# Performance work log

Hardware: AMD Instinct MI355X
Metric: run time of the kernel (lower is better)

The kernel has to match this reference:

```python
import jax, jax.numpy as jnp
import numpy as np

# Model / shape constants (match init_kwargs)
D_MODEL = 256
NHEAD = 8
H_B, W_B = 16, 8       # block_size
BN_H, BN_W = 8, 8      # block_num
B = 8
N = BN_H * H_B * BN_W * W_B  # 8192
HIDDEN = int(D_MODEL * 4.0)  # mlp_ratio * d_model
LN_EPS = 1e-5


def setup_inputs() -> dict:
    key = jax.random.key(0)
    ks = jax.random.split(key, 12)
    s = 0.02
    p = {}
    p["src"] = jax.random.normal(ks[0], (B, N, D_MODEL), jnp.float32)
    p["pos"] = jax.random.normal(ks[1], (1, N, D_MODEL), jnp.float32)
    # long-range MHA params (torch in_proj_weight [3C,C], out_proj [C,C])
    p["w_in_long"] = jax.random.normal(ks[2], (3 * D_MODEL, D_MODEL), jnp.float32) * s
    p["b_in_long"] = jnp.zeros((3 * D_MODEL,), jnp.float32)
    p["w_out_long"] = jax.random.normal(ks[3], (D_MODEL, D_MODEL), jnp.float32) * s
    p["b_out_long"] = jnp.zeros((D_MODEL,), jnp.float32)
    # short-range MHA params
    p["w_in_short"] = jax.random.normal(ks[4], (3 * D_MODEL, D_MODEL), jnp.float32) * s
    p["b_in_short"] = jnp.zeros((3 * D_MODEL,), jnp.float32)
    p["w_out_short"] = jax.random.normal(ks[5], (D_MODEL, D_MODEL), jnp.float32) * s
    p["b_out_short"] = jnp.zeros((D_MODEL,), jnp.float32)
    # FFN
    p["w1"] = jax.random.normal(ks[6], (HIDDEN, D_MODEL), jnp.float32) * s
    p["b1"] = jnp.zeros((HIDDEN,), jnp.float32)
    p["w2"] = jax.random.normal(ks[7], (D_MODEL, HIDDEN), jnp.float32) * s
    p["b2"] = jnp.zeros((D_MODEL,), jnp.float32)
    # LayerNorms
    p["g1"] = jnp.ones((D_MODEL,), jnp.float32)
    p["beta1"] = jnp.zeros((D_MODEL,), jnp.float32)
    p["g2"] = jnp.ones((D_MODEL,), jnp.float32)
    p["beta2"] = jnp.zeros((D_MODEL,), jnp.float32)
    return p


def _mha(q, k, v, w_in, b_in, w_out, b_out):
    # torch nn.MultiheadAttention, inputs [L, Bt, C] (seq-first)
    L, Bt, C = q.shape
    H, Dh = NHEAD, C // NHEAD
    wq, wk, wv = jnp.split(w_in, 3, axis=0)
    bq, bk, bv = jnp.split(b_in, 3, axis=0)
    qh = (q @ wq.T + bq).reshape(L, Bt, H, Dh)
    kh = (k @ wk.T + bk).reshape(L, Bt, H, Dh)
    vh = (v @ wv.T + bv).reshape(L, Bt, H, Dh)
    scores = jnp.einsum('lbhd,mbhd->bhlm', qh, kh) / np.sqrt(Dh).astype(np.float32)
    attn = jax.nn.softmax(scores, axis=-1)
    o = jnp.einsum('bhlm,mbhd->lbhd', attn, vh).reshape(L, Bt, C)
    return o @ w_out.T + b_out


def _ln(x, g, b):
    mu = jnp.mean(x, axis=-1, keepdims=True)
    var = jnp.var(x, axis=-1, keepdims=True)
    return (x - mu) / jnp.sqrt(var + LN_EPS) * g + b


def _isa_block(src, pos, w_in_long, b_in_long, w_out_long, b_out_long,
               w_in_short, b_in_short, w_out_short, b_out_short):
    Bs, Ns, C = src.shape
    posb = jnp.broadcast_to(pos, (Bs, Ns, C))

    def to_long(x):  # [B,N,C] -> [bn_h*bn_w, B*h_b*w_b, C]
        x = x.reshape(Bs, BN_H, H_B, BN_W, W_B, C).transpose(1, 3, 0, 2, 4, 5)
        return x.reshape(BN_H * BN_W, Bs * H_B * W_B, C)

    ql = to_long(src)
    pl = to_long(posb)
    v = _mha(ql + pl, ql + pl, ql, w_in_long, b_in_long, w_out_long, b_out_long)

    def long_to_short(x):
        # faithful to torch: view(B,bn_h,h_b,bn_w,w_b,C) REINTERPRETS the flat
        # (bn_h,bn_w,B,h_b,w_b) layout, then permute(2,4,0,1,3,5)
        x = x.reshape(Bs, BN_H, H_B, BN_W, W_B, C).transpose(2, 4, 0, 1, 3, 5)
        return x.reshape(H_B * W_B, Bs * BN_H * BN_W, C)

    v = long_to_short(v)
    ps = long_to_short(pl.reshape(Bs, BN_H, H_B, BN_W, W_B, C).reshape(BN_H * BN_W, Bs * H_B * W_B, C))
    # (the above reshape round-trip is identity; keep ps derived from pl directly)
    ps = long_to_short(pl)

    out = _mha(v + ps, v + ps, v, w_in_short, b_in_short, w_out_short, b_out_short)
    # [h_b*w_b, B*bn_h*bn_w, C] -> [B, N, C]
    out = out.reshape(H_B, W_B, Bs, BN_H, BN_W, C).transpose(2, 0, 3, 1, 4, 5)
    return out.reshape(Bs, Ns, C)


def reference(src, pos, w_in_long, b_in_long, w_out_long, b_out_long,
              w_in_short, b_in_short, w_out_short, b_out_short,
              w1, b1, w2, b2, g1, beta1, g2, beta2):
    Bs, Ns, C = src.shape
    src2 = _isa_block(src, pos, w_in_long, b_in_long, w_out_long, b_out_long,
                      w_in_short, b_in_short, w_out_short, b_out_short)
    x = src + src2            # dropout is identity at eval
    x = _ln(x, g1, beta1)
    ff = (jax.nn.relu(x @ w1.T + b1)) @ w2.T + b2
    x = _ln(x + ff, g2, beta2)
    # faithful final permute+view from the torch module (layout reinterpretation)
    x = jnp.transpose(x, (0, 2, 1)).reshape(Bs, Ns, C)
    return x
```

## Files before the change

### kernel.cpp

```cpp
#include <hip/hip_runtime.h>
#include <stdint.h>

typedef unsigned short u16;
typedef unsigned int u32;
typedef __bf16 bf16x8 __attribute__((ext_vector_type(8)));
typedef float f32x4 __attribute__((ext_vector_type(4)));

#define SC_Q 0.17677669529663687f

__device__ __forceinline__ u16 f2b(float f) {
  u32 u = __float_as_uint(f);
  u = (u + 0x7fffu + ((u >> 16) & 1u)) >> 16;
  return (u16)u;
}
__device__ __forceinline__ float b2f(u16 h) {
  return __uint_as_float(((u32)h) << 16);
}
__device__ __forceinline__ u32 pack2(float a, float b) {
  return (u32)f2b(a) | ((u32)f2b(b) << 16);
}
__device__ __forceinline__ void gload_lds16(const u16* g, u16* l) {
  __builtin_amdgcn_global_load_lds(
      (const __attribute__((address_space(1))) void*)g,
      (__attribute__((address_space(3))) void*)l, 16, 0, 0);
}

__global__ void prep_weights(const float* __restrict__ wil, const float* __restrict__ wol,
                             const float* __restrict__ wis, const float* __restrict__ wos,
                             const float* __restrict__ w1, const float* __restrict__ w2,
                             u16* __restrict__ out) {
  int idx = (blockIdx.x * 256 + threadIdx.x) * 4;
  u16 r[4];
#pragma unroll
  for (int j = 0; j < 4; ++j) {
    int i = idx + j;
    float x;
    if (i < 196608)      { x = wil[i]; if (i < 65536) x *= SC_Q; }
    else if (i < 262144) { x = wol[i - 196608]; }
    else if (i < 458752) { int k = i - 262144; x = wis[k]; if (k < 65536) x *= SC_Q; }
    else if (i < 524288) { x = wos[i - 458752]; }
    else if (i < 786432) { x = w1[i - 524288]; }
    else                 { x = w2[i - 786432]; }
    r[j] = f2b(x);
  }
  *(uint2*)(out + idx) = make_uint2((u32)r[0] | ((u32)r[1] << 16),
                                    (u32)r[2] | ((u32)r[3] << 16));
}

__global__ void prep_bias(const float* __restrict__ bil, const float* __restrict__ bis,
                          float* __restrict__ out) {
  int i = blockIdx.x * 256 + threadIdx.x;
  if (i < 768)       out[i] = bil[i] * (i < 256 ? SC_Q : 1.0f);
  else if (i < 1536) { int k = i - 768; out[i] = bis[k] * (k < 256 ? SC_Q : 1.0f); }
}

__global__ void gather_long(const float* __restrict__ src, const float* __restrict__ pos,
                            u16* __restrict__ A1, u16* __restrict__ A2) {
  int gid = blockIdx.x * 256 + threadIdx.x;
  int u = gid >> 6, lane = gid & 63;
  int l = u >> 10, t = u & 1023;
  int bh = l >> 3, bw = l & 7;
  int b = t >> 7, h = (t >> 3) & 15, w = t & 7;
  int n = bh * 1024 + h * 64 + bw * 8 + w;
  float4 s4 = ((const float4*)(src + ((size_t)b * 8192 + n) * 256))[lane];
  float4 p4 = ((const float4*)(pos + (size_t)n * 256))[lane];
  ((uint2*)(A1 + (size_t)u * 256))[lane] =
      make_uint2(pack2(s4.x + p4.x, s4.y + p4.y), pack2(s4.z + p4.z, s4.w + p4.w));
  ((uint2*)(A2 + (size_t)u * 256))[lane] =
      make_uint2(pack2(s4.x, s4.y), pack2(s4.z, s4.w));
}

__global__ void gather_short(const u16* __restrict__ VL, const float* __restrict__ pos,
                             u16* __restrict__ A1s, u16* __restrict__ A2s) {
  int gid = blockIdx.x * 256 + threadIdx.x;
  int u2 = gid >> 6, lane = gid & 63;
  int s = u2 >> 9, r = u2 & 511;
  int hq = s >> 3, wq = s & 7;
  int b = r >> 6, bh = (r >> 3) & 7, bw = r & 7;
  int u = b * 8192 + bh * 1024 + hq * 64 + bw * 8 + wq;
  int l = u >> 10, t = u & 1023;
  int pbh = l >> 3, pbw = l & 7, ph = (t >> 3) & 15, pw = t & 7;
  int np = pbh * 1024 + ph * 64 + pbw * 8 + pw;
  uint2 vv = ((const uint2*)(VL + (size_t)u * 256))[lane];
  float4 p4 = ((const float4*)(pos + (size_t)np * 256))[lane];
  float v0 = b2f((u16)(vv.x & 0xffff)), v1 = b2f((u16)(vv.x >> 16));
  float v2 = b2f((u16)(vv.y & 0xffff)), v3 = b2f((u16)(vv.y >> 16));
  ((uint2*)(A1s + (size_t)u2 * 256))[lane] =
      make_uint2(pack2(v0 + p4.x, v1 + p4.y), pack2(v2 + p4.z, v3 + p4.w));
  ((uint2*)(A2s + (size_t)u2 * 256))[lane] = vv;
}

__global__ __launch_bounds__(256) void gemm128(
    const u16* __restrict__ A1, const u16* __restrict__ A2, int n_split,
    const u16* __restrict__ W, const float* __restrict__ bias,
    u16* __restrict__ C, int N, int K, int relu) {
  __shared__ __align__(16) u16 As[128 * 32];
  __shared__ __align__(16) u16 Bs[128 * 32];
  int m0 = blockIdx.y * 128, n0 = blockIdx.x * 128;
  const u16* A = (n0 < n_split) ? A1 : A2;
  int tid = threadIdx.x;
  int lane = tid & 63, wv = tid >> 6;
  int row = tid >> 2, seg = tid & 3;
  int wr = wv & 1, wc = wv >> 1;
  int r15 = lane & 15, q = lane >> 4;
  f32x4 acc[4][4];
#pragma unroll
  for (int i = 0; i < 4; ++i)
#pragma unroll
    for (int j = 0; j < 4; ++j)
#pragma unroll
      for (int r = 0; r < 4; ++r) acc[i][j][r] = 0.f;

  const u16* ag0 = A + (size_t)(m0 + row) * K + seg * 8;
  const u16* ag1 = A + (size_t)(m0 + 64 + row) * K + seg * 8;
  const u16* bg0 = W + (size_t)(n0 + row) * K + seg * 8;
  const u16* bg1 = W + (size_t)(n0 + 64 + row) * K + seg * 8;
  u16* lA0 = As + wv * 512;
  u16* lA1 = As + wv * 512 + 2048;
  u16* lB0 = Bs + wv * 512;
  u16* lB1 = Bs + wv * 512 + 2048;

  for (int k0 = 0; k0 < K; k0 += 32) {
    gload_lds16(ag0 + k0, lA0);
    gload_lds16(ag1 + k0, lA1);
    gload_lds16(bg0 + k0, lB0);
    gload_lds16(bg1 + k0, lB1);
    __syncthreads();
    bf16x8 af[4], bf[4];
#pragma unroll
    for (int i = 0; i < 4; ++i)
      af[i] = *(const bf16x8*)&As[(wr * 64 + i * 16 + r15) * 32 + q * 8];
#pragma unroll
    for (int j = 0; j < 4; ++j)
      bf[j] = *(const bf16x8*)&Bs[(wc * 64 + j * 16 + r15) * 32 + q * 8];
#pragma unroll
    for (int i = 0; i < 4; ++i)
#pragma unroll
      for (int j = 0; j < 4; ++j)
        acc[i][j] = __builtin_amdgcn_mfma_f32_16x16x32_bf16(af[i], bf[j], acc[i][j], 0, 0, 0);
    __syncthreads();
  }
#pragma unroll
  for (int j = 0; j < 4; ++j) {
    int n = n0 + wc * 64 + j * 16 + r15;
    float bb = bias[n];
#pragma unroll
    for (int i = 0; i < 4; ++i)
#pragma unroll
      for (int r = 0; r < 4; ++r) {
        int m = m0 + wr * 64 + i * 16 + q * 4 + r;
        float v = acc[i][j][r] + bb;
        if (relu) v = fmaxf(v, 0.f);
        C[(size_t)m * N + n] = f2b(v);
      }
  }
}

template <int L, int Bt>
__global__ __launch_bounds__(4 * L) void attn_mfma(const u16* __restrict__ qkv,
                                                   u16* __restrict__ O) {
  constexpr int L16 = L / 16, LP = L + 8;
  __shared__ __align__(16) u16 Ks[L * 40];
  __shared__ __align__(16) u16 VT[32 * LP];
  __shared__ __align__(16) u16 Ps[L16 * 16 * LP];
  int p = blockIdx.x, t = p >> 3, head = p & 7;
  int tid = threadIdx.x;
  {
    int r = tid >> 2, seg = tid & 3;
    const u16* base = qkv + ((size_t)r * Bt + t) * 768 + head * 32 + seg * 8;
    uint4 kvv = *(const uint4*)(base + 256);
    *(uint4*)&Ks[r * 40 + seg * 8] = kvv;
    uint4 vv = *(const uint4*)(base + 512);
    u32 wds[4] = {vv.x, vv.y, vv.z, vv.w};
#pragma unroll
    for (int e = 0; e < 4; ++e) {
      VT[(seg * 8 + e * 2 + 0) * LP + r] = (u16)(wds[e] & 0xffffu);
      VT[(seg * 8 + e * 2 + 1) * LP + r] = (u16)(wds[e] >> 16);
    }
  }
  int lane = tid & 63, w = tid >> 6;
  int r15 = lane & 15, q = lane >> 4;
  bf16x8 af = *(const bf16x8*)(qkv + ((size_t)(w * 16 + r15) * Bt + t) * 768 + head * 32 + q * 8);
  __syncthreads();
  f32x4 z = {0.f, 0.f, 0.f, 0.f};
  f32x4 s[L16];
#pragma unroll
  for (int jt = 0; jt < L16; ++jt) {
    bf16x8 bf = *(const bf16x8*)&Ks[(jt * 16 + r15) * 40 + q * 8];
    s[jt] = __builtin_amdgcn_mfma_f32_16x16x32_bf16(af, bf, z, 0, 0, 0);
  }
  float inv[4];
#pragma unroll
  for (int r = 0; r < 4; ++r) {
    float mx = s[0][r];
#pragma unroll
    for (int jt = 1; jt < L16; ++jt) mx = fmaxf(mx, s[jt][r]);
    mx = fmaxf(mx, __shfl_xor(mx, 1));
    mx = fmaxf(mx, __shfl_xor(mx, 2));
    mx = fmaxf(mx, __shfl_xor(mx, 4));
    mx = fmaxf(mx, __shfl_xor(mx, 8));
    float sum = 0.f;
#pragma unroll
    for (int jt = 0; jt < L16; ++jt) {
      float pe = __expf(s[jt][r] - mx);
      s[jt][r] = pe;
      sum += pe;
    }
    sum += __shfl_xor(sum, 1);
    sum += __shfl_xor(sum, 2);
    sum += __shfl_xor(sum, 4);
    sum += __shfl_xor(sum, 8);
    inv[r] = 1.f / sum;
  }
  int pbase = w * 16 * LP;
#pragma unroll
  for (int jt = 0; jt < L16; ++jt)
#pragma unroll
    for (int r = 0; r < 4; ++r)
      Ps[pbase + (q * 4 + r) * LP + jt * 16 + r15] = f2b(s[jt][r]);
  __syncthreads();
  f32x4 o[2] = {z, z};
#pragma unroll
  for (int kt = 0; kt < L / 32; ++kt) {
    bf16x8 ap = *(const bf16x8*)&Ps[pbase + r15 * LP + kt * 32 + q * 8];
#pragma unroll
    for (int nt = 0; nt < 2; ++nt) {
      bf16x8 bv = *(const bf16x8*)&VT[(nt * 16 + r15) * LP + kt * 32 + q * 8];
      o[nt] = __builtin_amdgcn_mfma_f32_16x16x32_bf16(ap, bv, o[nt], 0, 0, 0);
    }
  }
#pragma unroll
  for (int nt = 0; nt < 2; ++nt)
#pragma unroll
    for (int r = 0; r < 4; ++r) {
      float v = o[nt][r] * inv[r];
      size_t addr = ((size_t)(w * 16 + q * 4 + r) * Bt + t) * 256 + head * 32 + nt * 16 + r15;
      O[addr] = f2b(v);
    }
}

__global__ void ln1(const float* __restrict__ src, const u16* __restrict__ s2b,
                    const float* __restrict__ g, const float* __restrict__ be,
                    u16* __restrict__ xln) {
  int gid = blockIdx.x * 256 + threadIdx.x;
  int u2 = gid >> 6, lane = gid & 63;
  int s = u2 >> 9, r = u2 & 511;
  int hq = s >> 3, wq = s & 7;
  int b = r >> 6, bh = (r >> 3) & 7, bw = r & 7;
  int n2 = hq * 512 + bh * 64 + wq * 8 + bw;
  size_t urow = (size_t)b * 8192 + n2;
  float4 a = ((const float4*)(src + urow * 256))[lane];
  uint2 vv = ((const uint2*)(s2b + (size_t)u2 * 256))[lane];
  float v0 = a.x + b2f((u16)(vv.x & 0xffff));
  float v1 = a.y + b2f((u16)(vv.x >> 16));
  float v2 = a.z + b2f((u16)(vv.y & 0xffff));
  float v3 = a.w + b2f((u16)(vv.y >> 16));
  float s1 = v0 + v1 + v2 + v3;
  float sq = v0*v0 + v1*v1 + v2*v2 + v3*v3;
#pragma unroll
  for (int off = 32; off >= 1; off >>= 1) {
    s1 += __shfl_xor(s1, off, 64);
    sq += __shfl_xor(sq, off, 64);
  }
  float mu = s1 * (1.f / 256.f);
  float var = sq * (1.f / 256.f) - mu * mu;
  float rstd = rsqrtf(var + 1e-5f);
  float4 g4 = ((const float4*)g)[lane];
  float4 e4 = ((const float4*)be)[lane];
  float y0 = (v0 - mu) * rstd * g4.x + e4.x;
  float y1 = (v1 - mu) * rstd * g4.y + e4.y;
  float y2 = (v2 - mu) * rstd * g4.z + e4.z;
  float y3 = (v3 - mu) * rstd * g4.w + e4.w;
  ((uint2*)(xln + urow * 256))[lane] = make_uint2(pack2(y0, y1), pack2(y2, y3));
}

__global__ __launch_bounds__(256) void ln2t(const u16* __restrict__ ff, const u16* __restrict__ xln,
                                            const float* __restrict__ g, const float* __restrict__ be,
                                            float* __restrict__ out) {
  __shared__ u16 tileT[256][65];
  __shared__ float ps1[64][4];
  __shared__ float ps2[64][4];
  __shared__ float mu_s[64], rs_s[64];
  int b = blockIdx.x >> 7;
  int n0 = (blockIdx.x & 127) * 64;
  int tid = threadIdx.x;
  int i = tid >> 2, ch = tid & 3;
  size_t u = (size_t)b * 8192 + n0 + i;
  const uint4* fr = (const uint4*)(ff + u * 256 + ch * 64);
  const uint4* xr = (const uint4*)(xln + u * 256 + ch * 64);
  float s1 = 0.f, sq = 0.f;
#pragma unroll
  for (int j = 0; j < 8; ++j) {
    uint4 fv = fr[j];
    uint4 xv = xr[j];
    u32 fw[4] = {fv.x, fv.y, fv.z, fv.w};
    u32 xw[4] = {xv.x, xv.y, xv.z, xv.w};
    int cbase = ch * 64 + j * 8;
#pragma unroll
    for (int e = 0; e < 4; ++e) {
      float f0 = __uint_as_float(fw[e] << 16) + __uint_as_float(xw[e] << 16);
      float f1 = __uint_as_float(fw[e] & 0xffff0000u) + __uint_as_float(xw[e] & 0xffff0000u);
      s1 += f0 + f1; sq += f0 * f0 + f1 * f1;
      tileT[cbase + e * 2 + 0][i] = f2b(f0);
      tileT[cbase + e * 2 + 1][i] = f2b(f1);
    }
  }
  ps1[i][ch] = s1; ps2[i][ch] = sq;
  __syncthreads();
  if (tid < 64) {
    float a1 = ps1[tid][0] + ps1[tid][1] + ps1[tid][2] + ps1[tid][3];
    float a2 = ps2[tid][0] + ps2[tid][1] + ps2[tid][2] + ps2[tid][3];
    float mu = a1 * (1.f / 256.f);
    float var = a2 * (1.f / 256.f) - mu * mu;
    mu_s[tid] = mu;
    rs_s[tid] = rsqrtf(var + 1e-5f);
  }
  __syncthreads();
  int ii = tid & 63, cq = tid >> 6;
  float mu = mu_s[ii], rs = rs_s[ii];
  float* ob = out + (size_t)b * 2097152 + n0 + ii;
#pragma unroll 4
  for (int pass = 0; pass < 64; ++pass) {
    int c = pass * 4 + cq;
    float val = b2f(tileT[c][ii]);
    float y = (val - mu) * rs * g[c] + be[c];
    ob[(size_t)c * 8192] = y;
  }
}

extern "C" void kernel_launch(void* const* d_in, const int* in_sizes, int n_in,
                              void* d_out, int out_size, void* d_ws, size_t ws_size,
                              hipStream_t stream) {
  (void)in_sizes; (void)n_in; (void)out_size; (void)ws_size;
  const float* src = (const float*)d_in[0];
  const float* pos = (const float*)d_in[1];
  const float* wil = (const float*)d_in[2];
  const float* bil = (const float*)d_in[3];
  const float* wol = (const float*)d_in[4];
  const float* bol = (const float*)d_in[5];
  const float* wis = (const float*)d_in[6];
  const float* bis = (const float*)d_in[7];
  const float* wos = (const float*)d_in[8];
  const float* bos = (const float*)d_in[9];
  const float* w1  = (const float*)d_in[10];
  const float* b1  = (const float*)d_in[11];
  const float* w2  = (const float*)d_in[12];
  const float* b2  = (const float*)d_in[13];
  const float* g1  = (const float*)d_in[14];
  const float* be1 = (const float*)d_in[15];
  const float* g2  = (const float*)d_in[16];
  const float* be2 = (const float*)d_in[17];

  char* ws = (char*)d_ws;
  u16* WB   = (u16*)ws;
  float* BS = (float*)(ws + (2ull << 20));
  u16* QKV  = (u16*)(ws + (4ull << 20));
  u16* R1   = (u16*)(ws + (100ull << 20));
  u16* R2   = (u16*)(ws + (132ull << 20));
  u16* R3   = (u16*)(ws + (164ull << 20));
  u16* H    = QKV;

  u16* wl_in  = WB;
  u16* wl_out = WB + 196608;
  u16* ws_in  = WB + 262144;
  u16* ws_out = WB + 458752;
  u16* w1b    = WB + 524288;
  u16* w2b    = WB + 786432;
  float* bsl = BS;
  float* bss = BS + 768;

  prep_weights<<<1024, 256, 0, stream>>>(wil, wol, wis, wos, w1, w2, WB);
  prep_bias<<<6, 256, 0, stream>>>(bil, bis, BS);
  gather_long<<<16384, 256, 0, stream>>>(src, pos, R1, R2);
  gemm128<<<dim3(6, 512), 256, 0, stream>>>(R1, R2, 512, wl_in, bsl, QKV, 768, 256, 0);
  attn_mfma<64, 1024><<<8192, 256, 0, stream>>>(QKV, R3);
  gemm128<<<dim3(2, 512), 256, 0, stream>>>(R3, R3, 1 << 30, wl_out, bol, R1, 256, 256, 0);
  gather_short<<<16384, 256, 0, stream>>>(R1, pos, R2, R3);
  gemm128<<<dim3(6, 512), 256, 0, stream>>>(R2, R3, 512, ws_in, bss, QKV, 768, 256, 0);
  attn_mfma<128, 512><<<4096, 512, 0, stream>>>(QKV, R1);
  gemm128<<<dim3(2, 512), 256, 0, stream>>>(R1, R1, 1 << 30, ws_out, bos, R2, 256, 256, 0);
  ln1<<<16384, 256, 0, stream>>>(src, R2, g1, be1, R3);
  gemm128<<<dim3(8, 512), 256, 0, stream>>>(R3, R3, 1 << 30, w1b, b1, H, 1024, 256, 1);
  gemm128<<<dim3(2, 512), 256, 0, stream>>>(H, H, 1 << 30, w2b, b2, R2, 256, 1024, 0);
  ln2t<<<1024, 256, 0, stream>>>(R2, R3, g2, be2, (float*)d_out);
}
```

Before: 595.7 us.

## Deepen GEMM K-tile to 64 with XOR-swizzled LDS and grouped block order

The GEMM now stages a 64-wide K slice per iteration instead of 32, which halves the number of barrier pairs per tile. LDS columns are XOR-swizzled by row to avoid bank conflicts on the wider rows. The grid is flattened and remapped so groups of 8 M-tiles sweep all N-tiles together, aiming for better L2 reuse of A rows. LDS use doubles to 32KB per block, which may lower occupancy.

Result: faster. 558.5 us (-6.3%).

```diff
diff --git a/kernel.cpp b/kernel.cpp
--- a/kernel.cpp
+++ b/kernel.cpp
@@ -90,19 +90,24 @@
   ((uint2*)(A2s + (size_t)u2 * 256))[lane] = vv;
 }
 
+template <int NT>
 __global__ __launch_bounds__(256) void gemm128(
     const u16* __restrict__ A1, const u16* __restrict__ A2, int n_split,
     const u16* __restrict__ W, const float* __restrict__ bias,
     u16* __restrict__ C, int N, int K, int relu) {
-  __shared__ __align__(16) u16 As[128 * 32];
-  __shared__ __align__(16) u16 Bs[128 * 32];
-  int m0 = blockIdx.y * 128, n0 = blockIdx.x * 128;
+  __shared__ __align__(16) u16 As[128 * 64];
+  __shared__ __align__(16) u16 Bs[128 * 64];
+  int L = blockIdx.x;
+  int mt = ((L >> 3) / NT) * 8 + (L & 7);
+  int nt = (L >> 3) % NT;
+  int m0 = mt * 128, n0 = nt * 128;
   const u16* A = (n0 < n_split) ? A1 : A2;
   int tid = threadIdx.x;
   int lane = tid & 63, wv = tid >> 6;
-  int row = tid >> 2, seg = tid & 3;
   int wr = wv & 1, wc = wv >> 1;
   int r15 = lane & 15, q = lane >> 4;
+  int rowt = tid >> 3;
+  int pc = (tid & 7) ^ (rowt & 7);
   f32x4 acc[4][4];
 #pragma unroll
   for (int i = 0; i < 4; ++i)
@@ -111,33 +116,37 @@
 #pragma unroll
       for (int r = 0; r < 4; ++r) acc[i][j][r] = 0.f;
 
-  const u16* ag0 = A + (size_t)(m0 + row) * K + seg * 8;
-  const u16* ag1 = A + (size_t)(m0 + 64 + row) * K + seg * 8;
-  const u16* bg0 = W + (size_t)(n0 + row) * K + seg * 8;
-  const u16* bg1 = W + (size_t)(n0 + 64 + row) * K + seg * 8;
-  u16* lA0 = As + wv * 512;
-  u16* lA1 = As + wv * 512 + 2048;
-  u16* lB0 = Bs + wv * 512;
-  u16* lB1 = Bs + wv * 512 + 2048;
-
-  for (int k0 = 0; k0 < K; k0 += 32) {
-    gload_lds16(ag0 + k0, lA0);
-    gload_lds16(ag1 + k0, lA1);
-    gload_lds16(bg0 + k0, lB0);
-    gload_lds16(bg1 + k0, lB1);
+  const u16* ag = A + (size_t)(m0 + rowt) * K + pc * 8;
+  const u16* bg = W + (size_t)(n0 + rowt) * K + pc * 8;
+  int xs = r15 & 7;
+
+  for (int k0 = 0; k0 < K; k0 += 64) {
+#pragma unroll
+    for (int g = 0; g < 4; ++g) {
+      gload_lds16(ag + (size_t)(g * 32) * K + k0, As + g * 2048 + wv * 512);
+      gload_lds16(bg + (size_t)(g * 32) * K + k0, Bs + g * 2048 + wv * 512);
+    }
     __syncthreads();
-    bf16x8 af[4], bf[4];
-#pragma unroll
-    for (int i = 0; i < 4; ++i)
-      af[i] = *(const bf16x8*)&As[(wr * 64 + i * 16 + r15) * 32 + q * 8];
-#pragma unroll
-    for (int j = 0; j < 4; ++j)
-      bf[j] = *(const bf16x8*)&Bs[(wc * 64 + j * 16 + r15) * 32 + q * 8];
-#pragma unroll
-    for (int i = 0; i < 4; ++i)
-#pragma unroll
-      for (int j = 0; j < 4; ++j)
-        acc[i][j] = __builtin_amdgcn_mfma_f32_16x16x32_bf16(af[i], bf[j], acc[i][j], 0, 0, 0);
+#pragma unroll
+    for (int kk = 0; kk < 2; ++kk) {
+      int co = ((kk * 4 + q) ^ xs) * 8;
+      bf16x8 af[4], bf[4];
+#pragma unroll
+      for (int i = 0; i < 4; ++i) {
+        int row = wr * 64 + i * 16 + r15;
+        af[i] = *(const bf16x8*)&As[row * 64 + co];
+      }
+#pragma unroll
+      for (int j = 0; j < 4; ++j) {
+        int row = wc * 64 + j * 16 + r15;
+        bf[j] = *(const bf16x8*)&Bs[row * 64 + co];
+      }
+#pragma unroll
+      for (int i = 0; i < 4; ++i)
+#pragma unroll
+        for (int j = 0; j < 4; ++j)
+          acc[i][j] = __builtin_amdgcn_mfma_f32_16x16x32_bf16(af[i], bf[j], acc[i][j], 0, 0, 0);
+    }
     __syncthreads();
   }
 #pragma unroll
@@ -372,15 +381,15 @@
   prep_weights<<<1024, 256, 0, stream>>>(wil, wol, wis, wos, w1, w2, WB);
   prep_bias<<<6, 256, 0, stream>>>(bil, bis, BS);
   gather_long<<<16384, 256, 0, stream>>>(src, pos, R1, R2);
-  gemm128<<<dim3(6, 512), 256, 0, stream>>>(R1, R2, 512, wl_in, bsl, QKV, 768, 256, 0);
+  gemm128<6><<<512 * 6, 256, 0, stream>>>(R1, R2, 512, wl_in, bsl, QKV, 768, 256, 0);
   attn_mfma<64, 1024><<<8192, 256, 0, stream>>>(QKV, R3);
-  gemm128<<<dim3(2, 512), 256, 0, stream>>>(R3, R3, 1 << 30, wl_out, bol, R1, 256, 256, 0);
+  gemm128<2><<<512 * 2, 256, 0, stream>>>(R3, R3, 1 << 30, wl_out, bol, R1, 256, 256, 0);
   gather_short<<<16384, 256, 0, stream>>>(R1, pos, R2, R3);
-  gemm128<<<dim3(6, 512), 256, 0, stream>>>(R2, R3, 512, ws_in, bss, QKV, 768, 256, 0);
+  gemm128<6><<<512 * 6, 256, 0, stream>>>(R2, R3, 512, ws_in, bss, QKV, 768, 256, 0);
   attn_mfma<128, 512><<<4096, 512, 0, stream>>>(QKV, R1);
-  gemm128<<<dim3(2, 512), 256, 0, stream>>>(R1, R1, 1 << 30, ws_out, bos, R2, 256, 256, 0);
+  gemm128<2><<<512 * 2, 256, 0, stream>>>(R1, R1, 1 << 30, ws_out, bos, R2, 256, 256, 0);
   ln1<<<16384, 256, 0, stream>>>(src, R2, g1, be1, R3);
-  gemm128<<<dim3(8, 512), 256, 0, stream>>>(R3, R3, 1 << 30, w1b, b1, H, 1024, 256, 1);
-  gemm128<<<dim3(2, 512), 256, 0, stream>>>(H, H, 1 << 30, w2b, b2, R2, 256, 1024, 0);
+  gemm128<8><<<512 * 8, 256, 0, stream>>>(R3, R3, 1 << 30, w1b, b1, H, 1024, 256, 1);
+  gemm128<2><<<512 * 2, 256, 0, stream>>>(H, H, 1 << 30, w2b, b2, R2, 256, 1024, 0);
   ln2t<<<1024, 256, 0, stream>>>(R2, R3, g2, be2, (float*)d_out);
 }
```
